# Optimization experiments

Measured on AMD Instinct MI355X. Metric: run time of the kernel, lower is better.

## Reference

```python
import jax, jax.numpy as jnp
import numpy as np

D = 512
E = 1024
LAMBDA_INIT = 0.05

def setup_inputs() -> dict:
    key = jax.random.key(0)
    ks = jax.random.split(key, 8)
    B, S = 4, 4096
    X = jax.random.normal(ks[0], (B, S, E), dtype=jnp.float32)
    Wq = jax.random.normal(ks[1], (2 * D, E), dtype=jnp.float32) / np.sqrt(E)
    bq = jnp.zeros((2 * D,), dtype=jnp.float32)
    Wk = jax.random.normal(ks[2], (2 * D, E), dtype=jnp.float32) / np.sqrt(E)
    bk = jnp.zeros((2 * D,), dtype=jnp.float32)
    Wv = jax.random.normal(ks[3], (D, E), dtype=jnp.float32) / np.sqrt(E)
    bv = jnp.zeros((D,), dtype=jnp.float32)
    lam = jax.random.normal(ks[4], (1,), dtype=jnp.float32)
    return {"X": X, "Wq": Wq, "bq": bq, "Wk": Wk, "bk": bk, "Wv": Wv, "bv": bv, "lam": lam}

def reference(X, Wq, bq, Wk, bk, Wv, bv, lam):
    # Linear projections (torch Linear: x @ W.T + b)
    Q = jnp.einsum('bse,fe->bsf', X, Wq) + bq   # [B,S,2d]
    K = jnp.einsum('bse,fe->bsf', X, Wk) + bk   # [B,S,2d]
    V = jnp.einsum('bse,de->bsd', X, Wv) + bv   # [B,S,d]
    Q1, Q2 = Q[..., :D], Q[..., D:]
    K1, K2 = K[..., :D], K[..., D:]
    s = 1.0 / np.sqrt(D)
    A1 = jnp.einsum('bqd,bkd->bqk', Q1, K1) * s  # [B,S,S]
    A2 = jnp.einsum('bqd,bkd->bqk', Q2, K2) * s
    P1 = jax.nn.softmax(A1, axis=-1)
    P2 = jax.nn.softmax(A2, axis=-1)
    lambda_ = jnp.exp(lam) + LAMBDA_INIT         # scalar [1]
    diff = P1 - lambda_ * P2
    return jnp.einsum('bqk,bkd->bqd', diff, V)   # [B,S,d]
```

## Files before the change

### kernel.cpp

```cpp
#include <hip/hip_runtime.h>
#include <cstdint>
#include <cstddef>

#define NB    4
#define SEQ   4096
#define EDIM  1024
#define DHEAD 512
#define NTOK  (NB * SEQ)
#define FQK   2048
#define FQKV  2560

typedef __bf16 bf16x8 __attribute__((ext_vector_type(8)));
typedef float  f32x4  __attribute__((ext_vector_type(4)));

#define WAITCNT(VM) asm volatile("s_waitcnt vmcnt(" #VM ") lgkmcnt(0)" ::: "memory")
#define LGKM0()     asm volatile("s_waitcnt lgkmcnt(0)" ::: "memory")
#define SCHED0()    __builtin_amdgcn_sched_barrier(0)
#define BAR()       __builtin_amdgcn_s_barrier()
#define PRIO1()     __builtin_amdgcn_s_setprio(1)
#define PRIO0()     __builtin_amdgcn_s_setprio(0)

__device__ __forceinline__ unsigned short f2bf(float f) {
  union { float f; unsigned int u; } v; v.f = f;
  return (unsigned short)((v.u + 0x7fffu + ((v.u >> 16) & 1u)) >> 16);
}

__device__ __forceinline__ void gld_lds16(const void* g, void* l) {
  __builtin_amdgcn_global_load_lds(
      (const __attribute__((address_space(1))) unsigned int*)g,
      (__attribute__((address_space(3))) unsigned int*)l, 16, 0, 0);
}

template <class Epi>
__device__ __forceinline__ void gemm_bt_core(
    const unsigned short* __restrict__ A, const unsigned short* __restrict__ B,
    int K, int lda, int ldb, int m0, int n0, Epi epi) {
  __shared__ __align__(16) unsigned short As[2][128 * 32];
  __shared__ __align__(16) unsigned short Bs[2][128 * 32];
  const int t = threadIdx.x;
  const int w = t >> 6;
  const int lane = t & 63;
  const int wr = w >> 1, wc = w & 1;
  const int l15 = lane & 15, c16 = lane >> 4, x3 = l15 & 3;

  f32x4 acc[4][4];
#pragma unroll
  for (int i = 0; i < 4; ++i)
#pragma unroll
    for (int j = 0; j < 4; ++j) acc[i][j] = f32x4{0.f, 0.f, 0.f, 0.f};

  const int c0 = w * 128 + lane;
  const int c1 = w * 128 + 64 + lane;
  const int r0 = c0 >> 2, s0 = (c0 & 3) ^ (r0 & 3);
  const int r1 = c1 >> 2, s1 = (c1 & 3) ^ (r1 & 3);
  const int o0 = (w * 128) * 8;
  const int o1 = (w * 128 + 64) * 8;
  const unsigned short* gA0 = A + (size_t)(m0 + r0) * lda + s0 * 8;
  const unsigned short* gA1 = A + (size_t)(m0 + r1) * lda + s1 * 8;
  const unsigned short* gB0 = B + (size_t)(n0 + r0) * ldb + s0 * 8;
  const unsigned short* gB1 = B + (size_t)(n0 + r1) * ldb + s1 * 8;

  auto STAGE = [&](int buf, int kt) {
    gld_lds16(gA0 + kt, &As[buf][o0]);
    gld_lds16(gA1 + kt, &As[buf][o1]);
    gld_lds16(gB0 + kt, &Bs[buf][o0]);
    gld_lds16(gB1 + kt, &Bs[buf][o1]);
  };

  STAGE(0, 0);
  const int NT = K >> 5;
  for (int tt = 0; tt < NT; ++tt) {
    const int cb = tt & 1;
    if (tt + 1 < NT) { STAGE(cb ^ 1, (tt + 1) * 32); WAITCNT(4); }
    else             { WAITCNT(0); }
    BAR();
    PRIO1();
    bf16x8 af[4], bfr[4];
#pragma unroll
    for (int tm = 0; tm < 4; ++tm) {
      int r = wr * 64 + tm * 16 + l15;
      af[tm] = *(const bf16x8*)&As[cb][r * 32 + ((c16 ^ x3) * 8)];
    }
#pragma unroll
    for (int tn = 0; tn < 4; ++tn) {
      int r = wc * 64 + tn * 16 + l15;
      bfr[tn] = *(const bf16x8*)&Bs[cb][r * 32 + ((c16 ^ x3) * 8)];
    }
#pragma unroll
    for (int tm = 0; tm < 4; ++tm)
#pragma unroll
      for (int tn = 0; tn < 4; ++tn)
        acc[tm][tn] = __builtin_amdgcn_mfma_f32_16x16x32_bf16(
            af[tm], bfr[tn], acc[tm][tn], 0, 0, 0);
    PRIO0();
    BAR();
  }
  epi(acc, wr, wc, lane);
}

__global__ void k_cvt_x(const float* __restrict__ X, unsigned short* __restrict__ Xb) {
  int i = blockIdx.x * blockDim.x + threadIdx.x;
  float4 v = ((const float4*)X)[i];
  ushort4 o;
  o.x = f2bf(v.x); o.y = f2bf(v.y); o.z = f2bf(v.z); o.w = f2bf(v.w);
  ((ushort4*)Xb)[i] = o;
}

__global__ void k_pack_w(const float* __restrict__ Wq, const float* __restrict__ Wk,
                         const float* __restrict__ Wv, unsigned short* __restrict__ Wb) {
  int i = blockIdx.x * blockDim.x + threadIdx.x;
  int idx = i * 4;
  int f = idx >> 10, e = idx & 1023;
  const float* src = (f < 1024) ? (Wq + (size_t)f * 1024)
                   : (f < 2048) ? (Wk + (size_t)(f - 1024) * 1024)
                                : (Wv + (size_t)(f - 2048) * 1024);
  float4 v = *(const float4*)(src + e);
  ushort4 o;
  o.x = f2bf(v.x); o.y = f2bf(v.y); o.z = f2bf(v.z); o.w = f2bf(v.w);
  ((ushort4*)Wb)[i] = o;
}

__global__ void k_pack_b(const float* __restrict__ bq, const float* __restrict__ bk,
                         const float* __restrict__ bv, float* __restrict__ bc) {
  int f = blockIdx.x * blockDim.x + threadIdx.x;
  if (f < FQKV)
    bc[f] = (f < 1024) ? bq[f] : (f < 2048) ? bk[f - 1024] : bv[f - 2048];
}

__global__ void k_zero_f(float* __restrict__ p) {
  int i = blockIdx.x * blockDim.x + threadIdx.x;
  p[i] = 0.f;
}

__global__ __launch_bounds__(256) void k_qk(const unsigned short* __restrict__ Xb,
                                            const unsigned short* __restrict__ Wb,
                                            const float* __restrict__ bc,
                                            unsigned short* __restrict__ QK) {
  const int m0 = blockIdx.y * 128, n0 = blockIdx.x * 128;
  gemm_bt_core(Xb, Wb, EDIM, EDIM, EDIM, m0, n0,
    [&](f32x4 (&acc)[4][4], int wr, int wc, int lane) {
#pragma unroll
      for (int tm = 0; tm < 4; ++tm)
#pragma unroll
        for (int tn = 0; tn < 4; ++tn) {
          int kc = n0 + wc * 64 + tn * 16 + (lane & 15);
          float bias = bc[kc];
#pragma unroll
          for (int i = 0; i < 4; ++i) {
            int q = m0 + wr * 64 + tm * 16 + (lane >> 4) * 4 + i;
            __bf16 h = (__bf16)(acc[tm][tn][i] + bias);
            QK[(size_t)q * FQK + kc] = *(const unsigned short*)&h;
          }
        }
    });
}

__global__ __launch_bounds__(256) void k_v(const unsigned short* __restrict__ Xb,
                                           const unsigned short* __restrict__ Wb,
                                           const float* __restrict__ bc,
                                           unsigned short* __restrict__ Vt) {
  const int b = blockIdx.z;
  const int m0 = blockIdx.y * 128;
  const int n0 = blockIdx.x * 128;
  const unsigned short* A = Wb + (size_t)2048 * EDIM;
  const unsigned short* B = Xb + (size_t)b * SEQ * EDIM;
  unsigned short* Vb = Vt + (size_t)b * DHEAD * SEQ;
  gemm_bt_core(A, B, EDIM, EDIM, EDIM, m0, n0,
    [&](f32x4 (&acc)[4][4], int wr, int wc, int lane) {
#pragma unroll
      for (int tm = 0; tm < 4; ++tm)
#pragma unroll
        for (int tn = 0; tn < 4; ++tn) {
          int s = n0 + wc * 64 + tn * 16 + (lane & 15);
#pragma unroll
          for (int i = 0; i < 4; ++i) {
            int d = m0 + wr * 64 + tm * 16 + (lane >> 4) * 4 + i;
            __bf16 h = (__bf16)(acc[tm][tn][i] + bc[2048 + d]);
            Vb[(size_t)d * SEQ + s] = *(const unsigned short*)&h;
          }
        }
    });
}

__global__ __launch_bounds__(512, 2) void k_scores8(const unsigned short* __restrict__ QK,
                                                    unsigned short* __restrict__ E_c,
                                                    float* __restrict__ ls, int b0) {
  __shared__ __align__(16) unsigned short LA[2][256 * 64];
  __shared__ __align__(16) unsigned short LB[2][256 * 64];
  const int z = blockIdx.z, rb = z >> 1, which = z & 1, b = b0 + rb;
  const int m0 = blockIdx.y * 256, n0 = blockIdx.x * 256;
  const unsigned short* Aq = QK + (size_t)b * SEQ * FQK + which * 512;
  const unsigned short* Bk = Aq + 1024;
  unsigned short* Eb = E_c + (size_t)z * SEQ * SEQ;
  float* lr = ls + (size_t)which * NTOK + (size_t)b * SEQ;
  const int t = threadIdx.x, w = t >> 6, lane = t & 63;
  const int wr = w >> 2, wc = w & 3;
  const int l15 = lane & 15, c16 = lane >> 4, x7 = l15 & 7;

  f32x4 acc[8][4];
#pragma unroll
  for (int i = 0; i < 8; ++i)
#pragma unroll
    for (int j = 0; j < 4; ++j) acc[i][j] = f32x4{0.f, 0.f, 0.f, 0.f};

  unsigned goffA[4], goffB[4]; int loff[4];
#pragma unroll
  for (int i = 0; i < 4; ++i) {
    int c = w * 64 + lane + 512 * i;
    int r = c >> 3;
    int sg = (c & 7) ^ (r & 7);
    goffA[i] = (unsigned)((m0 + r) * FQK + sg * 8);
    goffB[i] = (unsigned)((n0 + r) * FQK + sg * 8);
    loff[i] = (w * 64 + 512 * i) * 8;
  }

  auto STAGE = [&](int buf, int kh) {
#pragma unroll
    for (int i = 0; i < 4; ++i) gld_lds16(Aq + goffA[i] + kh, &LA[buf][loff[i]]);
#pragma unroll
    for (int i = 0; i < 4; ++i) gld_lds16(Bk + goffB[i] + kh, &LB[buf][loff[i]]);
  };

#define LDA_S(CB, R, KS) (*(const bf16x8*)&LA[CB][(R) * 64 + ((((KS) * 4 + c16) ^ x7) * 8)])
#define LDB_S(CB, R, KS) (*(const bf16x8*)&LB[CB][(R) * 64 + ((((KS) * 4 + c16) ^ x7) * 8)])

  STAGE(0, 0);
  WAITCNT(0);
  BAR();

  for (int kt = 0; kt < 8; ++kt) {
    const int cb = kt & 1;
    bf16x8 af[4][2], b0f[2][2], b1f[2][2];
    if (kt < 7) STAGE(cb ^ 1, (kt + 1) * 64);
#pragma unroll
    for (int tq = 0; tq < 4; ++tq)
#pragma unroll
      for (int ks = 0; ks < 2; ++ks)
        af[tq][ks] = LDA_S(cb, wr * 128 + tq * 16 + l15, ks);
#pragma unroll
    for (int tn = 0; tn < 2; ++tn)
#pragma unroll
      for (int ks = 0; ks < 2; ++ks)
        b0f[tn][ks] = LDB_S(cb, wc * 64 + tn * 16 + l15, ks);
    BAR(); LGKM0(); SCHED0();
    PRIO1();
#pragma unroll
    for (int tq = 0; tq < 4; ++tq)
#pragma unroll
      for (int tn = 0; tn < 2; ++tn)
#pragma unroll
        for (int ks = 0; ks < 2; ++ks)
          acc[tq][tn] = __builtin_amdgcn_mfma_f32_16x16x32_bf16(
              af[tq][ks], b0f[tn][ks], acc[tq][tn], 0, 0, 0);
    PRIO0();
    BAR();
#pragma unroll
    for (int tn = 0; tn < 2; ++tn)
#pragma unroll
      for (int ks = 0; ks < 2; ++ks)
        b1f[tn][ks] = LDB_S(cb, wc * 64 + (tn + 2) * 16 + l15, ks);
    BAR(); LGKM0(); SCHED0();
    PRIO1();
#pragma unroll
    for (int tq = 0; tq < 4; ++tq)
#pragma unroll
      for (int tn = 0; tn < 2; ++tn)
#pragma unroll
        for (int ks = 0; ks < 2; ++ks)
          acc[tq][tn + 2] = __builtin_amdgcn_mfma_f32_16x16x32_bf16(
              af[tq][ks], b1f[tn][ks], acc[tq][tn + 2], 0, 0, 0);
    PRIO0();
    BAR();
#pragma unroll
    for (int tq = 0; tq < 4; ++tq)
#pragma unroll
      for (int ks = 0; ks < 2; ++ks)
        af[tq][ks] = LDA_S(cb, wr * 128 + 64 + tq * 16 + l15, ks);
    BAR(); LGKM0(); SCHED0();
    PRIO1();
#pragma unroll
    for (int tq = 0; tq < 4; ++tq)
#pragma unroll
      for (int tn = 0; tn < 2; ++tn)
#pragma unroll
        for (int ks = 0; ks < 2; ++ks)
          acc[4 + tq][tn + 2] = __builtin_amdgcn_mfma_f32_16x16x32_bf16(
              af[tq][ks], b1f[tn][ks], acc[4 + tq][tn + 2], 0, 0, 0);
    PRIO0();
    BAR();
    PRIO1();
#pragma unroll
    for (int tq = 0; tq < 4; ++tq)
#pragma unroll
      for (int tn = 0; tn < 2; ++tn)
#pragma unroll
        for (int ks = 0; ks < 2; ++ks)
          acc[4 + tq][tn] = __builtin_amdgcn_mfma_f32_16x16x32_bf16(
              af[tq][ks], b0f[tn][ks], acc[4 + tq][tn], 0, 0, 0);
    PRIO0();
    if (kt < 7) WAITCNT(0);
    BAR();
  }
#undef LDA_S
#undef LDB_S

  const float scale = 0.04419417382415922f;
  float rs[8][4];
#pragma unroll
  for (int tm = 0; tm < 8; ++tm)
#pragma unroll
    for (int i = 0; i < 4; ++i) rs[tm][i] = 0.f;
#pragma unroll
  for (int tm = 0; tm < 8; ++tm)
#pragma unroll
    for (int tn = 0; tn < 4; ++tn) {
      int k = n0 + wc * 64 + tn * 16 + l15;
#pragma unroll
      for (int i = 0; i < 4; ++i) {
        int q = m0 + wr * 128 + tm * 16 + c16 * 4 + i;
        float e = __expf(acc[tm][tn][i] * scale);
        __bf16 h = (__bf16)e;
        Eb[(size_t)q * SEQ + k] = *(const unsigned short*)&h;
        rs[tm][i] += (float)h;
      }
    }
#pragma unroll
  for (int tm = 0; tm < 8; ++tm)
#pragma unroll
    for (int i = 0; i < 4; ++i) {
      float v = rs[tm][i];
      v += __shfl_xor(v, 1);
      v += __shfl_xor(v, 2);
      v += __shfl_xor(v, 4);
      v += __shfl_xor(v, 8);
      rs[tm][i] = v;
    }
  if (l15 == 0) {
#pragma unroll
    for (int tm = 0; tm < 8; ++tm)
#pragma unroll
      for (int i = 0; i < 4; ++i) {
        int q = m0 + wr * 128 + tm * 16 + c16 * 4 + i;
        atomicAdd(&lr[q], rs[tm][i]);
      }
  }
}

__global__ __launch_bounds__(512, 2) void k_pv8(const unsigned short* __restrict__ E_c,
                                                const unsigned short* __restrict__ Vt,
                                                float* __restrict__ O12, int b0) {
  __shared__ __align__(16) unsigned short LA[2][256 * 64];
  __shared__ __align__(16) unsigned short LB[2][128 * 64];
  const int z = blockIdx.z, b = b0 + (z >> 1);
  const int q0 = blockIdx.y * 256, n0 = blockIdx.x * 128;
  const unsigned short* Ae = E_c + (size_t)z * SEQ * SEQ;
  const unsigned short* Bv = Vt + (size_t)b * DHEAD * SEQ;
  float* Ob = O12 + (size_t)z * SEQ * DHEAD;
  const int t = threadIdx.x, w = t >> 6, lane = t & 63;
  const int wr = w >> 1, wc = w & 1;
  const int l15 = lane & 15, c16 = lane >> 4, x7 = l15 & 7;

  f32x4 acc[4][4];
#pragma unroll
  for (int i = 0; i < 4; ++i)
#pragma unroll
    for (int j = 0; j < 4; ++j) acc[i][j] = f32x4{0.f, 0.f, 0.f, 0.f};

  unsigned goffE[4], goffV[2]; int loffE[4], loffV[2];
#pragma unroll
  for (int i = 0; i < 4; ++i) {
    int c = w * 64 + lane + 512 * i;
    int r = c >> 3;
    int sg = (c & 7) ^ (r & 7);
    goffE[i] = (unsigned)((q0 + r) * SEQ + sg * 8);
    loffE[i] = (w * 64 + 512 * i) * 8;
  }
#pragma unroll
  for (int i = 0; i < 2; ++i) {
    int c = w * 64 + lane + 512 * i;
    int r = c >> 3;
    int sg = (c & 7) ^ (r & 7);
    goffV[i] = (unsigned)((n0 + r) * SEQ + sg * 8);
    loffV[i] = (w * 64 + 512 * i) * 8;
  }

  auto STAGE = [&](int buf, int kh) {
#pragma unroll
    for (int i = 0; i < 4; ++i) gld_lds16(Ae + goffE[i] + kh, &LA[buf][loffE[i]]);
#pragma unroll
    for (int i = 0; i < 2; ++i) gld_lds16(Bv + goffV[i] + kh, &LB[buf][loffV[i]]);
  };

#define LDA_P(CB, R, KS) (*(const bf16x8*)&LA[CB][(R) * 64 + ((((KS) * 4 + c16) ^ x7) * 8)])
#define LDB_P(CB, R, KS) (*(const bf16x8*)&LB[CB][(R) * 64 + ((((KS) * 4 + c16) ^ x7) * 8)])

  STAGE(0, 0);
  WAITCNT(0);
  BAR();

  for (int kt = 0; kt < 64; ++kt) {
    const int cb = kt & 1;
    bf16x8 af[4][2], b0f[2][2], b1f[2][2];
    if (kt < 63) STAGE(cb ^ 1, (kt + 1) * 64);
#pragma unroll
    for (int tq = 0; tq < 4; ++tq)
#pragma unroll
      for (int ks = 0; ks < 2; ++ks)
        af[tq][ks] = LDA_P(cb, wr * 64 + tq * 16 + l15, ks);
#pragma unroll
    for (int tn = 0; tn < 2; ++tn)
#pragma unroll
      for (int ks = 0; ks < 2; ++ks)
        b0f[tn][ks] = LDB_P(cb, wc * 64 + tn * 16 + l15, ks);
    BAR(); LGKM0(); SCHED0();
    PRIO1();
#pragma unroll
    for (int tq = 0; tq < 4; ++tq)
#pragma unroll
      for (int tn = 0; tn < 2; ++tn)
#pragma unroll
        for (int ks = 0; ks < 2; ++ks)
          acc[tq][tn] = __builtin_amdgcn_mfma_f32_16x16x32_bf16(
              af[tq][ks], b0f[tn][ks], acc[tq][tn], 0, 0, 0);
    PRIO0();
    BAR();
#pragma unroll
    for (int tn = 0; tn < 2; ++tn)
#pragma unroll
      for (int ks = 0; ks < 2; ++ks)
        b1f[tn][ks] = LDB_P(cb, wc * 64 + (tn + 2) * 16 + l15, ks);
    BAR(); LGKM0(); SCHED0();
    PRIO1();
#pragma unroll
    for (int tq = 0; tq < 4; ++tq)
#pragma unroll
      for (int tn = 0; tn < 2; ++tn)
#pragma unroll
        for (int ks = 0; ks < 2; ++ks)
          acc[tq][tn + 2] = __builtin_amdgcn_mfma_f32_16x16x32_bf16(
              af[tq][ks], b1f[tn][ks], acc[tq][tn + 2], 0, 0, 0);
    PRIO0();
    if (kt < 63) WAITCNT(0);
    BAR();
  }
#undef LDA_P
#undef LDB_P

#pragma unroll
  for (int tq = 0; tq < 4; ++tq)
#pragma unroll
    for (int tn = 0; tn < 4; ++tn) {
      int d = n0 + wc * 64 + tn * 16 + l15;
#pragma unroll
      for (int i = 0; i < 4; ++i) {
        int q = q0 + wr * 64 + tq * 16 + c16 * 4 + i;
        Ob[(size_t)q * DHEAD + d] = acc[tq][tn][i];
      }
    }
}

__global__ void k_combine(const float* __restrict__ O12, const float* __restrict__ ls,
                          const float* __restrict__ lam, float* __restrict__ out, int b0) {
  int i = blockIdx.x * blockDim.x + threadIdx.x;
  float lambda = expf(lam[0]) + 0.05f;
  int gq = i >> 7;
  int rb = gq >> 12;
  int q = gq & 4095;
  int dv = i & 127;
  int b = b0 + rb;
  float inv1 = 1.f / ls[(size_t)b * SEQ + q];
  float inv2 = lambda / ls[NTOK + (size_t)b * SEQ + q];
  size_t ai = (size_t)(rb * 2) * (SEQ * 128) + (size_t)q * 128 + dv;
  float4 a = ((const float4*)O12)[ai];
  float4 c = ((const float4*)O12)[ai + SEQ * 128];
  float4 r;
  r.x = a.x * inv1 - c.x * inv2;
  r.y = a.y * inv1 - c.y * inv2;
  r.z = a.z * inv1 - c.z * inv2;
  r.w = a.w * inv1 - c.w * inv2;
  ((float4*)out)[(size_t)(b * SEQ + q) * 128 + dv] = r;
}

extern "C" void kernel_launch(void* const* d_in, const int* in_sizes, int n_in,
                              void* d_out, int out_size, void* d_ws, size_t ws_size,
                              hipStream_t stream) {
  const float* X   = (const float*)d_in[0];
  const float* Wq  = (const float*)d_in[1];
  const float* bq  = (const float*)d_in[2];
  const float* Wk  = (const float*)d_in[3];
  const float* bk  = (const float*)d_in[4];
  const float* Wv  = (const float*)d_in[5];
  const float* bv  = (const float*)d_in[6];
  const float* lam = (const float*)d_in[7];
  float* out = (float*)d_out;

  char* ws = (char*)d_ws;
  size_t off = 0;
  auto alloc = [&](size_t b) { size_t r = off; off += (b + 255) & ~(size_t)255; return r; };
  unsigned short* Xb  = (unsigned short*)(ws + alloc((size_t)NTOK * EDIM * 2));
  unsigned short* Wb  = (unsigned short*)(ws + alloc((size_t)FQKV * EDIM * 2));
  float*          bc  = (float*)(ws + alloc((size_t)FQKV * 4));
  unsigned short* QK  = (unsigned short*)(ws + alloc((size_t)NTOK * FQK * 2));
  unsigned short* Vt  = (unsigned short*)(ws + alloc((size_t)NB * DHEAD * SEQ * 2));
  unsigned short* E_c = (unsigned short*)(ws + alloc((size_t)4 * SEQ * SEQ * 2));
  float*          ls  = (float*)(ws + alloc((size_t)2 * NTOK * 4));
  float* O12 = (float*)Xb;

  k_cvt_x<<<dim3((NTOK * EDIM / 4) / 256), dim3(256), 0, stream>>>(X, Xb);
  k_pack_w<<<dim3((FQKV * EDIM / 4) / 256), dim3(256), 0, stream>>>(Wq, Wk, Wv, Wb);
  k_pack_b<<<dim3(10), dim3(256), 0, stream>>>(bq, bk, bv, bc);
  k_qk<<<dim3(FQK / 128, NTOK / 128), dim3(256), 0, stream>>>(Xb, Wb, bc, QK);
  k_v<<<dim3(SEQ / 128, DHEAD / 128, NB), dim3(256), 0, stream>>>(Xb, Wb, bc, Vt);
  k_zero_f<<<dim3(2 * NTOK / 256), dim3(256), 0, stream>>>(ls);
  for (int b0 = 0; b0 < NB; b0 += 2) {
    k_scores8<<<dim3(SEQ / 256, SEQ / 256, 4), dim3(512), 0, stream>>>(QK, E_c, ls, b0);
    k_pv8<<<dim3(DHEAD / 128, SEQ / 256, 4), dim3(512), 0, stream>>>(E_c, Vt, O12, b0);
    k_combine<<<dim3((2 * SEQ * DHEAD / 4) / 256), dim3(256), 0, stream>>>(O12, ls, lam, out, b0);
  }

  (void)in_sizes; (void)n_in; (void)out_size; (void)ws_size;
}
```

Before: 734.1 us.

## Interleave QK staging loads with MFMA phases and simplify PV loop

The score GEMM kernel now issues the next K-tile's global-to-LDS loads in pieces across the four MFMA phases, and waits on partial vmcnt counts instead of draining everything at the end of each iteration. The PV kernel's loop is collapsed into one phase: it stages the next tile, waits with a partial vmcnt, loads all A and B fragments, and runs all MFMAs between only two barriers. The aim is to hide global load latency and cut barrier and wait overhead. The risk is that the partial vmcnt counts must exactly match the issue order, or the code reads LDS data before it has arrived.

```diff
diff --git a/kernel.cpp b/kernel.cpp
--- a/kernel.cpp
+++ b/kernel.cpp
@@ -214,24 +214,22 @@
     loff[i] = (w * 64 + 512 * i) * 8;
   }
 
-  auto STAGE = [&](int buf, int kh) {
-#pragma unroll
-    for (int i = 0; i < 4; ++i) gld_lds16(Aq + goffA[i] + kh, &LA[buf][loff[i]]);
-#pragma unroll
-    for (int i = 0; i < 4; ++i) gld_lds16(Bk + goffB[i] + kh, &LB[buf][loff[i]]);
-  };
+  auto stgA = [&](int buf, int i, int kh) { gld_lds16(Aq + goffA[i] + kh, &LA[buf][loff[i]]); };
+  auto stgB = [&](int buf, int i, int kh) { gld_lds16(Bk + goffB[i] + kh, &LB[buf][loff[i]]); };
 
 #define LDA_S(CB, R, KS) (*(const bf16x8*)&LA[CB][(R) * 64 + ((((KS) * 4 + c16) ^ x7) * 8)])
 #define LDB_S(CB, R, KS) (*(const bf16x8*)&LB[CB][(R) * 64 + ((((KS) * 4 + c16) ^ x7) * 8)])
 
-  STAGE(0, 0);
-  WAITCNT(0);
+  stgB(0, 0, 0); stgB(0, 1, 0); stgB(0, 2, 0); stgB(0, 3, 0);
+  stgA(0, 0, 0); stgA(0, 2, 0); stgA(0, 1, 0); stgA(0, 3, 0);
+  WAITCNT(2);
   BAR();
 
   for (int kt = 0; kt < 8; ++kt) {
-    const int cb = kt & 1;
+    const int cb = kt & 1, nb = cb ^ 1;
+    const int kh = (kt + 1) * 64;
     bf16x8 af[4][2], b0f[2][2], b1f[2][2];
-    if (kt < 7) STAGE(cb ^ 1, (kt + 1) * 64);
+
 #pragma unroll
     for (int tq = 0; tq < 4; ++tq)
 #pragma unroll
@@ -242,6 +240,7 @@
 #pragma unroll
       for (int ks = 0; ks < 2; ++ks)
         b0f[tn][ks] = LDB_S(cb, wc * 64 + tn * 16 + l15, ks);
+    if (kt < 7) { stgB(nb, 0, kh); stgB(nb, 1, kh); }
     BAR(); LGKM0(); SCHED0();
     PRIO1();
 #pragma unroll
@@ -254,11 +253,13 @@
               af[tq][ks], b0f[tn][ks], acc[tq][tn], 0, 0, 0);
     PRIO0();
     BAR();
+
 #pragma unroll
     for (int tn = 0; tn < 2; ++tn)
 #pragma unroll
       for (int ks = 0; ks < 2; ++ks)
         b1f[tn][ks] = LDB_S(cb, wc * 64 + (tn + 2) * 16 + l15, ks);
+    if (kt < 7) { stgB(nb, 2, kh); stgB(nb, 3, kh); }
     BAR(); LGKM0(); SCHED0();
     PRIO1();
 #pragma unroll
@@ -270,12 +271,15 @@
           acc[tq][tn + 2] = __builtin_amdgcn_mfma_f32_16x16x32_bf16(
               af[tq][ks], b1f[tn][ks], acc[tq][tn + 2], 0, 0, 0);
     PRIO0();
-    BAR();
+    if (kt < 7) WAITCNT(4); else WAITCNT(0);
+    BAR();
+
 #pragma unroll
     for (int tq = 0; tq < 4; ++tq)
 #pragma unroll
       for (int ks = 0; ks < 2; ++ks)
         af[tq][ks] = LDA_S(cb, wr * 128 + 64 + tq * 16 + l15, ks);
+    if (kt < 7) { stgA(nb, 0, kh); stgA(nb, 2, kh); }
     BAR(); LGKM0(); SCHED0();
     PRIO1();
 #pragma unroll
@@ -288,6 +292,8 @@
               af[tq][ks], b1f[tn][ks], acc[4 + tq][tn + 2], 0, 0, 0);
     PRIO0();
     BAR();
+
+    if (kt < 7) { stgA(nb, 1, kh); stgA(nb, 3, kh); }
     PRIO1();
 #pragma unroll
     for (int tq = 0; tq < 4; ++tq)
@@ -298,7 +304,7 @@
           acc[4 + tq][tn] = __builtin_amdgcn_mfma_f32_16x16x32_bf16(
               af[tq][ks], b0f[tn][ks], acc[4 + tq][tn], 0, 0, 0);
     PRIO0();
-    if (kt < 7) WAITCNT(0);
+    if (kt < 7) WAITCNT(2);
     BAR();
   }
 #undef LDA_S
@@ -391,60 +397,37 @@
     for (int i = 0; i < 2; ++i) gld_lds16(Bv + goffV[i] + kh, &LB[buf][loffV[i]]);
   };
 
-#define LDA_P(CB, R, KS) (*(const bf16x8*)&LA[CB][(R) * 64 + ((((KS) * 4 + c16) ^ x7) * 8)])
-#define LDB_P(CB, R, KS) (*(const bf16x8*)&LB[CB][(R) * 64 + ((((KS) * 4 + c16) ^ x7) * 8)])
-
   STAGE(0, 0);
-  WAITCNT(0);
-  BAR();
-
   for (int kt = 0; kt < 64; ++kt) {
     const int cb = kt & 1;
-    bf16x8 af[4][2], b0f[2][2], b1f[2][2];
-    if (kt < 63) STAGE(cb ^ 1, (kt + 1) * 64);
-#pragma unroll
-    for (int tq = 0; tq < 4; ++tq)
+    if (kt < 63) { STAGE(cb ^ 1, (kt + 1) * 64); WAITCNT(6); }
+    else         { WAITCNT(0); }
+    BAR();
+    PRIO1();
+    bf16x8 af[4][2], bfr[4][2];
+#pragma unroll
+    for (int tn = 0; tn < 4; ++tn)
 #pragma unroll
       for (int ks = 0; ks < 2; ++ks)
-        af[tq][ks] = LDA_P(cb, wr * 64 + tq * 16 + l15, ks);
-#pragma unroll
-    for (int tn = 0; tn < 2; ++tn)
+        bfr[tn][ks] = *(const bf16x8*)
+            &LB[cb][(wc * 64 + tn * 16 + l15) * 64 + (((ks * 4 + c16) ^ x7) * 8)];
+#pragma unroll
+    for (int tq = 0; tq < 4; ++tq)
 #pragma unroll
       for (int ks = 0; ks < 2; ++ks)
-        b0f[tn][ks] = LDB_P(cb, wc * 64 + tn * 16 + l15, ks);
-    BAR(); LGKM0(); SCHED0();
-    PRIO1();
-#pragma unroll
-    for (int tq = 0; tq < 4; ++tq)
-#pragma unroll
-      for (int tn = 0; tn < 2; ++tn)
+        af[tq][ks] = *(const bf16x8*)
+            &LA[cb][(wr * 64 + tq * 16 + l15) * 64 + (((ks * 4 + c16) ^ x7) * 8)];
+#pragma unroll
+    for (int tq = 0; tq < 4; ++tq)
+#pragma unroll
+      for (int tn = 0; tn < 4; ++tn)
 #pragma unroll
         for (int ks = 0; ks < 2; ++ks)
           acc[tq][tn] = __builtin_amdgcn_mfma_f32_16x16x32_bf16(
-              af[tq][ks], b0f[tn][ks], acc[tq][tn], 0, 0, 0);
+              af[tq][ks], bfr[tn][ks], acc[tq][tn], 0, 0, 0);
     PRIO0();
     BAR();
-#pragma unroll
-    for (int tn = 0; tn < 2; ++tn)
-#pragma unroll
-      for (int ks = 0; ks < 2; ++ks)
-        b1f[tn][ks] = LDB_P(cb, wc * 64 + (tn + 2) * 16 + l15, ks);
-    BAR(); LGKM0(); SCHED0();
-    PRIO1();
-#pragma unroll
-    for (int tq = 0; tq < 4; ++tq)
-#pragma unroll
-      for (int tn = 0; tn < 2; ++tn)
-#pragma unroll
-        for (int ks = 0; ks < 2; ++ks)
-          acc[tq][tn + 2] = __builtin_amdgcn_mfma_f32_16x16x32_bf16(
-              af[tq][ks], b1f[tn][ks], acc[tq][tn + 2], 0, 0, 0);
-    PRIO0();
-    if (kt < 63) WAITCNT(0);
-    BAR();
-  }
-#undef LDA_P
-#undef LDB_P
+  }
 
 #pragma unroll
   for (int tq = 0; tq < 4; ++tq)
```

Result: faster. 684.0 us (-6.8%).
